# Kernel tuning notes

Measured on AMD Instinct MI355X. Metric: run time of the kernel, lower is better.

Reference implementation:

```python
import jax, jax.numpy as jnp
import numpy as np

DIM = 128
HEADS = 4
DH = 32
SCALE = DH ** -0.5


def _ln(x, g, b):
    m = x.mean(-1, keepdims=True)
    v = x.var(-1, keepdims=True)
    return (x - m) / jnp.sqrt(v + 1e-5) * g + b


def setup_inputs() -> dict:
    key = jax.random.key(0)
    ks = jax.random.split(key, 16)
    B, N, H, W, HK, WK = 2, 6, 48, 48, 24, 24
    d, hd = DIM, HEADS * DH
    p = lambda k, s: (jax.random.normal(k, s, jnp.float32) * 0.02)
    return {
        "q": jax.random.normal(ks[0], (B, N, d, H, W), jnp.float32),
        "k": jax.random.normal(ks[1], (B, N, d, HK, WK), jnp.float32),
        "v": jax.random.normal(ks[2], (B, N, d, HK, WK), jnp.float32),
        "skip": jax.random.normal(ks[3], (B, d, H, W), jnp.float32),
        "lnq_g": jnp.ones(d), "lnq_b": jnp.zeros(d),
        "Wq": p(ks[4], (d, hd)), "bq": jnp.zeros(hd),
        "lnk_g": jnp.ones(d), "lnk_b": jnp.zeros(d),
        "Wk": p(ks[5], (d, hd)), "bk": jnp.zeros(hd),
        "lnv_g": jnp.ones(d), "lnv_b": jnp.zeros(d),
        "Wv": p(ks[6], (d, hd)), "bv": jnp.zeros(hd),
        "Wp": p(ks[7], (hd, d)), "bp": jnp.zeros(d),
        "pre_g": jnp.ones(d), "pre_b": jnp.zeros(d),
        "W1": p(ks[8], (d, 2 * d)), "b1": jnp.zeros(2 * d),
        "W2": p(ks[9], (2 * d, d)), "b2": jnp.zeros(d),
        "post_g": jnp.ones(d), "post_b": jnp.zeros(d),
    }


def reference(q, k, v, skip, lnq_g, lnq_b, Wq, bq, lnk_g, lnk_b, Wk, bk,
              lnv_g, lnv_b, Wv, bv, Wp, bp, pre_g, pre_b, W1, b1, W2, b2,
              post_g, post_b):
    B, N, d, H, W = q.shape
    _, _, _, HK, WK = k.shape
    Q, K = H * W, HK * WK
    # b n d H W -> b n (H W) d
    qx = q.transpose(0, 1, 3, 4, 2).reshape(B, N, Q, d)
    kx = k.transpose(0, 1, 3, 4, 2).reshape(B, N, K, d)
    vx = v.transpose(0, 1, 3, 4, 2).reshape(B, N * K, d)
    # norm + linear projections
    qp = _ln(qx, lnq_g, lnq_b) @ Wq + bq  # (B,N,Q,HEADS*DH)
    kp = _ln(kx, lnk_g, lnk_b) @ Wk + bk
    vp = _ln(vx, lnv_g, lnv_b) @ Wv + bv  # (B,N*K,HEADS*DH)
    # split heads: b ... (m d) -> (b m) ... d
    qp = qp.reshape(B, N, Q, HEADS, DH).transpose(0, 3, 1, 2, 4).reshape(B * HEADS, N, Q, DH)
    kp = kp.reshape(B, N, K, HEADS, DH).transpose(0, 3, 1, 2, 4).reshape(B * HEADS, N, K, DH)
    vp = vp.reshape(B, N * K, HEADS, DH).transpose(0, 2, 1, 3).reshape(B * HEADS, N * K, DH)
    # per-view scores, then softmax jointly over (n K)
    scores = SCALE * jnp.einsum('bnqd,bnkd->bnqk', qp, kp)
    scores = scores.transpose(0, 2, 1, 3).reshape(B * HEADS, Q, N * K)
    a = jax.nn.softmax(scores, axis=-1)
    out = jnp.einsum('bqk,bkd->bqd', a, vp)  # (B*HEADS, Q, DH)
    # merge heads: (b m) Q d -> b Q (m d)
    z = out.reshape(B, HEADS, Q, DH).transpose(0, 2, 1, 3).reshape(B, Q, HEADS * DH)
    z = z @ Wp + bp
    z = z + skip.transpose(0, 2, 3, 1).reshape(B, Q, d)
    z = _ln(z, pre_g, pre_b)
    z = z + (jax.nn.gelu(z @ W1 + b1, approximate=False) @ W2 + b2)
    z = _ln(z, post_g, post_b)
    return z.reshape(B, H, W, d).transpose(0, 3, 1, 2)
```

## Files before the change

### kernel.cpp

```cpp
#include <hip/hip_runtime.h>
#include <cmath>

#define B_    2
#define N_    6
#define D_    128
#define Q_    2304
#define K_    576
#define NK_   3456
#define HEADS_ 4
#define DH_   32
#define SCALE_ 0.17677669529663687f
#define SCLOG2E_ 0.25504672615621814f

typedef __attribute__((ext_vector_type(8))) short bf16x8;
typedef __attribute__((ext_vector_type(4))) float f32x4;

#if defined(__has_builtin)
#if __has_builtin(__builtin_amdgcn_cvt_pk_bf16_f32)
#define HAS_PK_BF16 1
#endif
#endif

static __device__ __forceinline__ unsigned short f2bf(float f) {
  union { float f; unsigned u; } x; x.f = f;
  unsigned u = x.u + 0x7fffu + ((x.u >> 16) & 1u);
  return (unsigned short)(u >> 16);
}
static __device__ __forceinline__ unsigned pkbf(float a, float b) {
#ifdef HAS_PK_BF16
  typedef __attribute__((ext_vector_type(2))) __bf16 vbf2;
  union { vbf2 v; unsigned u; } cv;
  cv.v = __builtin_amdgcn_cvt_pk_bf16_f32(a, b);
  return cv.u;
#else
  return (unsigned)f2bf(a) | ((unsigned)f2bf(b) << 16);
#endif
}

static __device__ __forceinline__ void pl32sw(unsigned &a, unsigned &b) {
  asm("v_permlane32_swap_b32 %0, %1" : "+v"(a), "+v"(b));
}
static __device__ __forceinline__ void pl16sw(unsigned &a, unsigned &b) {
  asm("v_permlane16_swap_b32 %0, %1" : "+v"(a), "+v"(b));
}

__global__ __launch_bounds__(256) void k_prep_wt(
    const float* __restrict__ Wq, const float* __restrict__ Wk,
    const float* __restrict__ Wv, const float* __restrict__ Wp,
    const float* __restrict__ W1, const float* __restrict__ W2,
    unsigned short* __restrict__ WTq, unsigned short* __restrict__ WTk,
    unsigned short* __restrict__ WTv, unsigned short* __restrict__ WTp,
    unsigned short* __restrict__ WT1, unsigned short* __restrict__ WT2,
    float* __restrict__ Z, int zn)
{
  __shared__ float tile[32][33];
  const int wb = blockIdx.x, t = threadIdx.x;
  {
    const float4 z4 = {0.f, 0.f, 0.f, 0.f};
    for (int i = wb * 256 + t; i < zn; i += 128 * 256)
      ((float4*)Z)[i] = z4;
  }
  const float* src; unsigned short* dst; int Kd, J, tl;
  if      (wb < 16) { src = Wq; dst = WTq; Kd = 128; J = 128; tl = wb; }
  else if (wb < 32) { src = Wk; dst = WTk; Kd = 128; J = 128; tl = wb - 16; }
  else if (wb < 48) { src = Wv; dst = WTv; Kd = 128; J = 128; tl = wb - 32; }
  else if (wb < 64) { src = Wp; dst = WTp; Kd = 128; J = 128; tl = wb - 48; }
  else if (wb < 96) { src = W1; dst = WT1; Kd = 128; J = 256; tl = wb - 64; }
  else              { src = W2; dst = WT2; Kd = 256; J = 128; tl = wb - 96; }
  const int njt = J >> 5;
  const int tj = tl % njt, tk = tl / njt;
#pragma unroll
  for (int i = 0; i < 4; ++i) {
    int idx = t + 256 * i;
    int r = idx >> 5, c = idx & 31;
    tile[r][c] = src[(size_t)(tk * 32 + r) * J + tj * 32 + c];
  }
  __syncthreads();
#pragma unroll
  for (int i = 0; i < 2; ++i) {
    int idx = t + 256 * i;
    int rr = idx >> 4, c2 = (idx & 15) << 1;
    *(unsigned*)&dst[(size_t)(tj * 32 + rr) * Kd + tk * 32 + c2] =
        pkbf(tile[c2][rr], tile[c2 + 1][rr]);
  }
}

__global__ __launch_bounds__(256) void k_ln_proj_all(
    const float* __restrict__ qin, const float* __restrict__ kin,
    const float* __restrict__ vin,
    const float* __restrict__ lnq_g, const float* __restrict__ lnq_b,
    const float* __restrict__ lnk_g, const float* __restrict__ lnk_b,
    const float* __restrict__ lnv_g, const float* __restrict__ lnv_b,
    const unsigned short* __restrict__ WTq, const unsigned short* __restrict__ WTk,
    const unsigned short* __restrict__ WTv,
    const float* __restrict__ bq, const float* __restrict__ bk,
    const float* __restrict__ bv,
    unsigned short* __restrict__ QPh, unsigned short* __restrict__ KPh,
    unsigned short* __restrict__ VPTh)
{
  __shared__ float xs[32][132];
  __shared__ unsigned short xh[32][136];
  __shared__ float gs[128], bs[128];
  __shared__ float mu[32], rsd[32];
  const int t = threadIdx.x;
  const int bid = blockIdx.x;

  const float* x; const unsigned short* WT; const float* g; const float* bl;
  const float* bias; int S, blk, mode; float osc;
  if (bid < 864)       { mode = 0; blk = bid;        x = qin; WT = WTq; g = lnq_g; bl = lnq_b; bias = bq; S = Q_; osc = SCLOG2E_; }
  else if (bid < 1080) { mode = 0; blk = bid - 864;  x = kin; WT = WTk; g = lnk_g; bl = lnk_b; bias = bk; S = K_; osc = 1.0f; }
  else                 { mode = 1; blk = bid - 1080; x = vin; WT = WTv; g = lnv_g; bl = lnv_b; bias = bv; S = K_; osc = 1.0f; }
  const int ntile = S >> 5;
  const int o  = blk / ntile;
  const int s0 = (blk % ntile) << 5;

  if (t < 128) { gs[t] = g[t]; bs[t] = bl[t]; }
  const float* xb = x + (size_t)o * 128 * (size_t)S + s0;
#pragma unroll
  for (int i = 0; i < 4; ++i) {
    int idx = t + 256 * i;
    int c = idx >> 3, s4 = (idx & 7) << 2;
    float4 xv = *(const float4*)&xb[(size_t)c * S + s4];
    xs[s4 + 0][c] = xv.x; xs[s4 + 1][c] = xv.y;
    xs[s4 + 2][c] = xv.z; xs[s4 + 3][c] = xv.w;
  }
  __syncthreads();
  {
    int s = t >> 3, l8 = t & 7;
    float sum = 0.f, sq = 0.f;
    for (int c = l8; c < 128; c += 8) { float v = xs[s][c]; sum += v; sq += v * v; }
#pragma unroll
    for (int off = 4; off > 0; off >>= 1) {
      sum += __shfl_down(sum, off, 8);
      sq  += __shfl_down(sq,  off, 8);
    }
    if (l8 == 0) {
      float mth = sum * 0.0078125f;
      float var = sq * 0.0078125f - mth * mth;
      mu[s] = mth; rsd[s] = rsqrtf(var + 1e-5f);
    }
  }
  __syncthreads();
#pragma unroll
  for (int i = 0; i < 8; ++i) {
    int idx = t + 256 * i;
    int s = idx >> 6, c2 = (idx & 63) << 1;
    float y0 = (xs[s][c2]     - mu[s]) * rsd[s] * gs[c2]     + bs[c2];
    float y1 = (xs[s][c2 + 1] - mu[s]) * rsd[s] * gs[c2 + 1] + bs[c2 + 1];
    *(unsigned*)&xh[s][c2] = pkbf(y0, y1);
  }
  __syncthreads();
  const int w = t >> 6, lane = t & 63, quad = lane >> 4, l16 = lane & 15;
  const f32x4 zf = {0.f, 0.f, 0.f, 0.f};
  f32x4 acc[2][2] = {{zf, zf}, {zf, zf}};
#pragma unroll
  for (int kc = 0; kc < 4; ++kc) {
    bf16x8 a0 = *(const bf16x8*)&xh[l16][kc * 32 + quad * 8];
    bf16x8 a1 = *(const bf16x8*)&xh[16 + l16][kc * 32 + quad * 8];
    bf16x8 b0 = *(const bf16x8*)&WT[(size_t)(w * 32 + l16) * 128 + kc * 32 + quad * 8];
    bf16x8 b1 = *(const bf16x8*)&WT[(size_t)(w * 32 + 16 + l16) * 128 + kc * 32 + quad * 8];
    acc[0][0] = __builtin_amdgcn_mfma_f32_16x16x32_bf16(a0, b0, acc[0][0], 0, 0, 0);
    acc[0][1] = __builtin_amdgcn_mfma_f32_16x16x32_bf16(a0, b1, acc[0][1], 0, 0, 0);
    acc[1][0] = __builtin_amdgcn_mfma_f32_16x16x32_bf16(a1, b0, acc[1][0], 0, 0, 0);
    acc[1][1] = __builtin_amdgcn_mfma_f32_16x16x32_bf16(a1, b1, acc[1][1], 0, 0, 0);
  }
  if (mode == 0) {
    unsigned short* outh = (bid < 864) ? QPh : KPh;
    __syncthreads();
#pragma unroll
    for (int mt = 0; mt < 2; ++mt)
#pragma unroll
      for (int nt = 0; nt < 2; ++nt) {
        int col = w * 32 + nt * 16 + l16;
        float bc = bias[col];
#pragma unroll
        for (int r = 0; r < 4; ++r)
          xh[mt * 16 + quad * 4 + r][col] = f2bf((acc[mt][nt][r] + bc) * osc);
      }
    __syncthreads();
#pragma unroll
    for (int i = 0; i < 2; ++i) {
      int s = i * 16 + (t >> 4), c8 = (t & 15) << 3;
      *(uint4*)&outh[((size_t)o * S + s0 + s) * 128 + c8] = *(uint4*)&xh[s][c8];
    }
  } else {
    const int b = o / 6, n = o % 6;
#pragma unroll
    for (int mt = 0; mt < 2; ++mt)
#pragma unroll
      for (int nt = 0; nt < 2; ++nt) {
        int col = w * 32 + nt * 16 + l16;
        int hh = col >> 5, dh = col & 31;
        float bc = bias[col];
        ushort4 pk;
        *(unsigned*)&pk.x = pkbf(acc[mt][nt][0] + bc, acc[mt][nt][1] + bc);
        *(unsigned*)&pk.z = pkbf(acc[mt][nt][2] + bc, acc[mt][nt][3] + bc);
        int s = n * 576 + s0 + mt * 16 + quad * 4;
        *(ushort4*)&VPTh[((size_t)(b * 4 + hh) * 32 + dh) * (size_t)NK_ + s] = pk;
      }
  }
}

__global__ __launch_bounds__(256) void k_attn_mfma(
    const unsigned short* __restrict__ QPh, const unsigned short* __restrict__ KPh,
    const unsigned short* __restrict__ VPTh, float* __restrict__ PO,
    float* __restrict__ Pl)
{
  __shared__ __align__(16) unsigned short smem[2][2048];
  const int t = threadIdx.x;
  const int w = t >> 6, lane = t & 63;
  const int quad = lane >> 4, l16 = lane & 15;
  const int qg  = blockIdx.x % 18;
  const int rest = blockIdx.x / 18;
  const int bhx = rest & 7, nn = rest >> 3;
  const int bb = bhx >> 2, h = bhx & 3;
  const int q0 = (qg * 4 + w) << 5;

  const unsigned short* kb = KPh + ((size_t)(bb * 6 + nn) * K_) * 128 + h * 32;
  const unsigned short* qb = QPh + ((size_t)(bb * 6 + nn) * Q_ + q0) * 128 + h * 32;
  const unsigned short* vb = VPTh + (size_t)bhx * 32 * (size_t)NK_ + (size_t)nn * 18 * 32;

  bf16x8 qc0 = *(const bf16x8*)&qb[(size_t)l16 * 128 + quad * 8];
  bf16x8 qc1 = *(const bf16x8*)&qb[(size_t)(16 + l16) * 128 + quad * 8];

  const int row16 = l16 + ((w & 1) << 4);
  const int xsl = (quad ^ ((l16 >> 1) & 3)) << 3;
  const unsigned short* sbase = (w < 2)
      ? kb + (size_t)row16 * 128 + quad * 8
      : vb + (size_t)row16 * NK_ + quad * 8;
  const int sstride = (w < 2) ? 4096 : 32;
  const int wdst = ((w >= 2) ? 1024 : 0) + row16 * 32 + xsl;

  const f32x4 zf = {0.f, 0.f, 0.f, 0.f};
  f32x4 o00 = zf, o01 = zf, o10 = zf, o11 = zf;
  float lsum0 = 0.f, lsum1 = 0.f;

  uint4 st0 = *(const uint4*)&sbase[0];
  uint4 stn = *(const uint4*)&sbase[sstride];
  *(uint4*)&smem[0][wdst] = st0;
  __syncthreads();

#pragma unroll 2
  for (int kc = 0; kc < 18; ++kc) {
    const int buf = kc & 1;
    if (kc < 17) *(uint4*)&smem[buf ^ 1][wdst] = stn;
    if (kc < 16) stn = *(const uint4*)&sbase[(size_t)(kc + 2) * sstride];

    const unsigned short* sb = &smem[buf][0];
    bf16x8 kf0 = *(const bf16x8*)&sb[l16 * 32 + xsl];
    bf16x8 kf1 = *(const bf16x8*)&sb[(16 + l16) * 32 + xsl];
    bf16x8 pv0 = *(const bf16x8*)&sb[1024 + l16 * 32 + xsl];
    bf16x8 pv1 = *(const bf16x8*)&sb[1024 + (16 + l16) * 32 + xsl];

    __builtin_amdgcn_s_setprio(1);
    f32x4 s00 = __builtin_amdgcn_mfma_f32_16x16x32_bf16(kf0, qc0, zf, 0, 0, 0);
    f32x4 s01 = __builtin_amdgcn_mfma_f32_16x16x32_bf16(kf1, qc0, zf, 0, 0, 0);
    f32x4 s10 = __builtin_amdgcn_mfma_f32_16x16x32_bf16(kf0, qc1, zf, 0, 0, 0);
    f32x4 s11 = __builtin_amdgcn_mfma_f32_16x16x32_bf16(kf1, qc1, zf, 0, 0, 0);

    float a00 = __builtin_amdgcn_exp2f(s00.x), a01 = __builtin_amdgcn_exp2f(s00.y);
    float a02 = __builtin_amdgcn_exp2f(s00.z), a03 = __builtin_amdgcn_exp2f(s00.w);
    float a10 = __builtin_amdgcn_exp2f(s01.x), a11 = __builtin_amdgcn_exp2f(s01.y);
    float a12 = __builtin_amdgcn_exp2f(s01.z), a13 = __builtin_amdgcn_exp2f(s01.w);
    lsum0 += (a00 + a01 + a02 + a03) + (a10 + a11 + a12 + a13);
    float b00 = __builtin_amdgcn_exp2f(s10.x), b01 = __builtin_amdgcn_exp2f(s10.y);
    float b02 = __builtin_amdgcn_exp2f(s10.z), b03 = __builtin_amdgcn_exp2f(s10.w);
    float b10 = __builtin_amdgcn_exp2f(s11.x), b11 = __builtin_amdgcn_exp2f(s11.y);
    float b12 = __builtin_amdgcn_exp2f(s11.z), b13 = __builtin_amdgcn_exp2f(s11.w);
    lsum1 += (b00 + b01 + b02 + b03) + (b10 + b11 + b12 + b13);

    unsigned xA0 = pkbf(a00, a01), xA1 = pkbf(a02, a03);
    unsigned xB0 = pkbf(a10, a11), xB1 = pkbf(a12, a13);
    unsigned yA0 = pkbf(b00, b01), yA1 = pkbf(b02, b03);
    unsigned yB0 = pkbf(b10, b11), yB1 = pkbf(b12, b13);
    pl32sw(xA0, xB0); pl32sw(xA1, xB1);
    pl16sw(xA0, xB0); pl16sw(xA1, xB1);
    pl32sw(yA0, yB0); pl32sw(yA1, yB1);
    pl16sw(yA0, yB0); pl16sw(yA1, yB1);
    union { unsigned u[4]; bf16x8 v; } f0, f1;
    f0.u[0] = xA0; f0.u[1] = xA1; f0.u[2] = xB0; f0.u[3] = xB1;
    f1.u[0] = yA0; f1.u[1] = yA1; f1.u[2] = yB0; f1.u[3] = yB1;

    o00 = __builtin_amdgcn_mfma_f32_16x16x32_bf16(f0.v, pv0, o00, 0, 0, 0);
    o01 = __builtin_amdgcn_mfma_f32_16x16x32_bf16(f0.v, pv1, o01, 0, 0, 0);
    o10 = __builtin_amdgcn_mfma_f32_16x16x32_bf16(f1.v, pv0, o10, 0, 0, 0);
    o11 = __builtin_amdgcn_mfma_f32_16x16x32_bf16(f1.v, pv1, o11, 0, 0, 0);
    __builtin_amdgcn_s_setprio(0);
    __syncthreads();
  }

  lsum0 += __shfl_xor(lsum0, 16);
  lsum0 += __shfl_xor(lsum0, 32);
  lsum1 += __shfl_xor(lsum1, 16);
  lsum1 += __shfl_xor(lsum1, 32);
  if (lane < 16) {
    atomicAdd(&Pl[(size_t)bhx * Q_ + q0 + lane], lsum0);
    atomicAdd(&Pl[(size_t)bhx * Q_ + q0 + 16 + lane], lsum1);
  }
  float* pob = PO + ((size_t)bhx * Q_ + q0) * 32;
#pragma unroll
  for (int r = 0; r < 4; ++r) {
    atomicAdd(&pob[(quad * 4 + r) * 32 + l16],           o00[r]);
    atomicAdd(&pob[(quad * 4 + r) * 32 + 16 + l16],      o01[r]);
    atomicAdd(&pob[(16 + quad * 4 + r) * 32 + l16],      o10[r]);
    atomicAdd(&pob[(16 + quad * 4 + r) * 32 + 16 + l16], o11[r]);
  }
}

__global__ __launch_bounds__(512) void k_tail(
    const float* __restrict__ PO, const float* __restrict__ Pl,
    const unsigned short* __restrict__ WTp, const float* __restrict__ bp,
    const float* __restrict__ skip,
    const float* __restrict__ pre_g, const float* __restrict__ pre_b,
    const unsigned short* __restrict__ WT1, const float* __restrict__ b1,
    const unsigned short* __restrict__ WT2, const float* __restrict__ b2,
    const float* __restrict__ post_g, const float* __restrict__ post_b,
    float* __restrict__ out)
{
  __shared__ float xs[16][132];
  __shared__ unsigned short xh[16][136];
  __shared__ unsigned short hb[16][264];
  __shared__ float g1s[128], b1s[128], g2s[128], b2s[128];
  __shared__ float mu[16], rsd[16];
  const int t = threadIdx.x;
  const int row0 = blockIdx.x << 4;
  const int bb = row0 / Q_, hw0 = row0 % Q_;
  const int w = t >> 6, lane = t & 63, quad = lane >> 4, l16 = lane & 15;
  const f32x4 zf = {0.f, 0.f, 0.f, 0.f};

  if (t < 128) { g1s[t] = pre_g[t]; b1s[t] = pre_b[t]; g2s[t] = post_g[t]; b2s[t] = post_b[t]; }
#pragma unroll
  for (int i = 0; i < 2; ++i) {
    int idx = t + 512 * i;
    int s = idx >> 6, c2 = (idx & 63) << 1;
    int q = hw0 + s;
    int h = c2 >> 5, dh = c2 & 31;
    size_t bq = (size_t)(bb * 4 + h) * Q_ + q;
    size_t i0 = bq * 32 + dh;
    float2 pp = *(const float2*)&PO[i0];
    float inv = 1.f / Pl[bq];
    *(unsigned*)&xh[s][c2] = pkbf(pp.x * inv, pp.y * inv);
  }
  __syncthreads();
  {
    f32x4 acc = zf;
    const int col = w * 16 + l16;
#pragma unroll
    for (int kc = 0; kc < 4; ++kc) {
      bf16x8 a0 = *(const bf16x8*)&xh[l16][kc * 32 + quad * 8];
      bf16x8 b0 = *(const bf16x8*)&WTp[(size_t)col * 128 + kc * 32 + quad * 8];
      acc = __builtin_amdgcn_mfma_f32_16x16x32_bf16(a0, b0, acc, 0, 0, 0);
    }
    float bc = bp[col];
    float4 sk = *(const float4*)&skip[((size_t)bb * 128 + col) * Q_ + hw0 + quad * 4];
    xs[quad * 4 + 0][col] = acc[0] + bc + sk.x;
    xs[quad * 4 + 1][col] = acc[1] + bc + sk.y;
    xs[quad * 4 + 2][col] = acc[2] + bc + sk.z;
    xs[quad * 4 + 3][col] = acc[3] + bc + sk.w;
  }
  __syncthreads();
  {
    int s = t >> 5, lg = t & 31;
    float sum = 0.f, sq = 0.f;
    for (int c = lg; c < 128; c += 32) { float v = xs[s][c]; sum += v; sq += v * v; }
#pragma unroll
    for (int off = 16; off > 0; off >>= 1) {
      sum += __shfl_down(sum, off, 32);
      sq  += __shfl_down(sq,  off, 32);
    }
    if (lg == 0) {
      float mth = sum * 0.0078125f;
      float var = sq * 0.0078125f - mth * mth;
      mu[s] = mth; rsd[s] = rsqrtf(var + 1e-5f);
    }
  }
  __syncthreads();
#pragma unroll
  for (int i = 0; i < 2; ++i) {
    int idx = t + 512 * i;
    int s = idx >> 6, c2 = (idx & 63) << 1;
    float y0 = (xs[s][c2]     - mu[s]) * rsd[s] * g1s[c2]     + b1s[c2];
    float y1 = (xs[s][c2 + 1] - mu[s]) * rsd[s] * g1s[c2 + 1] + b1s[c2 + 1];
    xs[s][c2] = y0; xs[s][c2 + 1] = y1;
    *(unsigned*)&xh[s][c2] = pkbf(y0, y1);
  }
  __syncthreads();
  {
#pragma unroll
    for (int nt = 0; nt < 2; ++nt) {
      const int col = w * 32 + nt * 16 + l16;
      f32x4 acc = zf;
#pragma unroll
      for (int kc = 0; kc < 4; ++kc) {
        bf16x8 a0 = *(const bf16x8*)&xh[l16][kc * 32 + quad * 8];
        bf16x8 b0 = *(const bf16x8*)&WT1[(size_t)col * 128 + kc * 32 + quad * 8];
        acc = __builtin_amdgcn_mfma_f32_16x16x32_bf16(a0, b0, acc, 0, 0, 0);
      }
      float bc = b1[col];
#pragma unroll
      for (int r = 0; r < 4; ++r) {
        float hx = acc[r] + bc;
        hb[quad * 4 + r][col] =
            f2bf(0.5f * hx * (1.f + erff(hx * 0.7071067811865476f)));
      }
    }
  }
  __syncthreads();
  {
    f32x4 acc = zf;
    const int col = w * 16 + l16;
#pragma unroll
    for (int kc = 0; kc < 8; ++kc) {
      bf16x8 a0 = *(const bf16x8*)&hb[l16][kc * 32 + quad * 8];
      bf16x8 b0 = *(const bf16x8*)&WT2[(size_t)col * 256 + kc * 32 + quad * 8];
      acc = __builtin_amdgcn_mfma_f32_16x16x32_bf16(a0, b0, acc, 0, 0, 0);
    }
    float bc = b2[col];
#pragma unroll
    for (int r = 0; r < 4; ++r) {
      int row = quad * 4 + r;
      xs[row][col] = acc[r] + bc + xs[row][col];
    }
  }
  __syncthreads();
  {
    int s = t >> 5, lg = t & 31;
    float sum = 0.f, sq = 0.f;
    for (int c = lg; c < 128; c += 32) { float v = xs[s][c]; sum += v; sq += v * v; }
#pragma unroll
    for (int off = 16; off > 0; off >>= 1) {
      sum += __shfl_down(sum, off, 32);
      sq  += __shfl_down(sq,  off, 32);
    }
    if (lg == 0) {
      float mth = sum * 0.0078125f;
      float var = sq * 0.0078125f - mth * mth;
      mu[s] = mth; rsd[s] = rsqrtf(var + 1e-5f);
    }
  }
  __syncthreads();
#pragma unroll
  for (int i = 0; i < 4; ++i) {
    int idx = t + 512 * i;
    int s = idx & 15, c = idx >> 4;
    out[(size_t)bb * (128 * (size_t)Q_) + (size_t)c * Q_ + hw0 + s] =
        (xs[s][c] - mu[s]) * rsd[s] * g2s[c] + b2s[c];
  }
}

extern "C" void kernel_launch(void* const* d_in, const int* in_sizes, int n_in,
                              void* d_out, int out_size, void* d_ws, size_t ws_size,
                              hipStream_t stream) {
  const float* q     = (const float*)d_in[0];
  const float* k     = (const float*)d_in[1];
  const float* v     = (const float*)d_in[2];
  const float* skip  = (const float*)d_in[3];
  const float* lnq_g = (const float*)d_in[4];
  const float* lnq_b = (const float*)d_in[5];
  const float* Wq    = (const float*)d_in[6];
  const float* bq    = (const float*)d_in[7];
  const float* lnk_g = (const float*)d_in[8];
  const float* lnk_b = (const float*)d_in[9];
  const float* Wk    = (const float*)d_in[10];
  const float* bk    = (const float*)d_in[11];
  const float* lnv_g = (const float*)d_in[12];
  const float* lnv_b = (const float*)d_in[13];
  const float* Wv    = (const float*)d_in[14];
  const float* bvv   = (const float*)d_in[15];
  const float* Wp    = (const float*)d_in[16];
  const float* bp    = (const float*)d_in[17];
  const float* pre_g = (const float*)d_in[18];
  const float* pre_b = (const float*)d_in[19];
  const float* W1    = (const float*)d_in[20];
  const float* b1    = (const float*)d_in[21];
  const float* W2    = (const float*)d_in[22];
  const float* b2    = (const float*)d_in[23];
  const float* post_g= (const float*)d_in[24];
  const float* post_b= (const float*)d_in[25];
  float* out = (float*)d_out;

  unsigned short* QPh  = (unsigned short*)d_ws;
  unsigned short* KPh  = QPh + 3538944;
  unsigned short* VPTh = KPh + 884736;
  float* PO  = (float*)(VPTh + 884736);
  float* Pl  = PO + 589824;
  unsigned short* WTq = (unsigned short*)(Pl + 18432);
  unsigned short* WTk = WTq + 16384;
  unsigned short* WTv = WTk + 16384;
  unsigned short* WTp = WTv + 16384;
  unsigned short* WT1 = WTp + 16384;
  unsigned short* WT2 = WT1 + 32768;
  const int zn = (589824 + 18432) / 4;

  k_prep_wt<<<dim3(128), dim3(256), 0, stream>>>(Wq, Wk, Wv, Wp, W1, W2,
                                                 WTq, WTk, WTv, WTp, WT1, WT2,
                                                 PO, zn);
  k_ln_proj_all<<<dim3(1296), dim3(256), 0, stream>>>(
      q, k, v, lnq_g, lnq_b, lnk_g, lnk_b, lnv_g, lnv_b,
      WTq, WTk, WTv, bq, bk, bvv, QPh, KPh, VPTh);
  k_attn_mfma<<<dim3(18 * 8 * 6), dim3(256), 0, stream>>>(QPh, KPh, VPTh, PO, Pl);
  k_tail<<<dim3(288), dim3(512), 0, stream>>>(PO, Pl, WTp, bp, skip,
                                              pre_g, pre_b, WT1, b1, WT2, b2,
                                              post_g, post_b, out);
}
```

Before: 165.0 us.

## Replace atomic partial-sum accumulation with per-view partial buffers reduced in tail

After: 167.2 us. About the same (+1.4%).

```diff
diff --git a/kernel.cpp b/kernel.cpp
--- a/kernel.cpp
+++ b/kernel.cpp
@@ -50,16 +50,10 @@
     const float* __restrict__ W1, const float* __restrict__ W2,
     unsigned short* __restrict__ WTq, unsigned short* __restrict__ WTk,
     unsigned short* __restrict__ WTv, unsigned short* __restrict__ WTp,
-    unsigned short* __restrict__ WT1, unsigned short* __restrict__ WT2,
-    float* __restrict__ Z, int zn)
+    unsigned short* __restrict__ WT1, unsigned short* __restrict__ WT2)
 {
   __shared__ float tile[32][33];
   const int wb = blockIdx.x, t = threadIdx.x;
-  {
-    const float4 z4 = {0.f, 0.f, 0.f, 0.f};
-    for (int i = wb * 256 + t; i < zn; i += 128 * 256)
-      ((float4*)Z)[i] = z4;
-  }
   const float* src; unsigned short* dst; int Kd, J, tl;
   if      (wb < 16) { src = Wq; dst = WTq; Kd = 128; J = 128; tl = wb; }
   else if (wb < 32) { src = Wk; dst = WTk; Kd = 128; J = 128; tl = wb - 16; }
@@ -206,7 +200,9 @@
     const unsigned short* __restrict__ VPTh, float* __restrict__ PO,
     float* __restrict__ Pl)
 {
-  __shared__ __align__(16) unsigned short smem[2][2048];
+  __shared__ __align__(16) char smem_u[18432];
+  unsigned short (*smem)[2048] = (unsigned short (*)[2048])smem_u;
+  float (*ol)[32][36] = (float (*)[32][36])smem_u;
   const int t = threadIdx.x;
   const int w = t >> 6, lane = t & 63;
   const int quad = lane >> 4, l16 = lane & 15;
@@ -294,16 +290,26 @@
   lsum1 += __shfl_xor(lsum1, 16);
   lsum1 += __shfl_xor(lsum1, 32);
   if (lane < 16) {
-    atomicAdd(&Pl[(size_t)bhx * Q_ + q0 + lane], lsum0);
-    atomicAdd(&Pl[(size_t)bhx * Q_ + q0 + 16 + lane], lsum1);
-  }
-  float* pob = PO + ((size_t)bhx * Q_ + q0) * 32;
+    float* plb = Pl + (size_t)(nn * 8 + bhx) * Q_ + q0;
+    plb[lane]      = lsum0;
+    plb[16 + lane] = lsum1;
+  }
 #pragma unroll
   for (int r = 0; r < 4; ++r) {
-    atomicAdd(&pob[(quad * 4 + r) * 32 + l16],           o00[r]);
-    atomicAdd(&pob[(quad * 4 + r) * 32 + 16 + l16],      o01[r]);
-    atomicAdd(&pob[(16 + quad * 4 + r) * 32 + l16],      o10[r]);
-    atomicAdd(&pob[(16 + quad * 4 + r) * 32 + 16 + l16], o11[r]);
+    ol[w][quad * 4 + r][l16]           = o00[r];
+    ol[w][quad * 4 + r][16 + l16]      = o01[r];
+    ol[w][16 + quad * 4 + r][l16]      = o10[r];
+    ol[w][16 + quad * 4 + r][16 + l16] = o11[r];
+  }
+  __syncthreads();
+  {
+    float* pob = PO + (size_t)(nn * 8 + bhx) * (Q_ * 32) + (size_t)qg * (128 * 32);
+    const int qr = t >> 1, d0 = (t & 1) << 4;
+#pragma unroll
+    for (int j = 0; j < 4; ++j) {
+      float4 vv = *(const float4*)&ol[qr >> 5][qr & 31][d0 + j * 4];
+      *(float4*)&pob[(size_t)t * 16 + j * 4] = vv;
+    }
   }
 }
 
@@ -337,9 +343,15 @@
     int h = c2 >> 5, dh = c2 & 31;
     size_t bq = (size_t)(bb * 4 + h) * Q_ + q;
     size_t i0 = bq * 32 + dh;
-    float2 pp = *(const float2*)&PO[i0];
-    float inv = 1.f / Pl[bq];
-    *(unsigned*)&xh[s][c2] = pkbf(pp.x * inv, pp.y * inv);
+    float px = 0.f, py = 0.f, l = 0.f;
+#pragma unroll
+    for (int p = 0; p < 6; ++p) {
+      float2 pp = *(const float2*)&PO[(size_t)p * 589824 + i0];
+      px += pp.x; py += pp.y;
+      l += Pl[(size_t)p * 18432 + bq];
+    }
+    float inv = 1.f / l;
+    *(unsigned*)&xh[s][c2] = pkbf(px * inv, py * inv);
   }
   __syncthreads();
   {
@@ -483,18 +495,16 @@
   unsigned short* KPh  = QPh + 3538944;
   unsigned short* VPTh = KPh + 884736;
   float* PO  = (float*)(VPTh + 884736);
-  float* Pl  = PO + 589824;
-  unsigned short* WTq = (unsigned short*)(Pl + 18432);
+  float* Pl  = PO + (size_t)6 * 589824;
+  unsigned short* WTq = (unsigned short*)(Pl + (size_t)6 * 18432);
   unsigned short* WTk = WTq + 16384;
   unsigned short* WTv = WTk + 16384;
   unsigned short* WTp = WTv + 16384;
   unsigned short* WT1 = WTp + 16384;
   unsigned short* WT2 = WT1 + 32768;
-  const int zn = (589824 + 18432) / 4;
 
   k_prep_wt<<<dim3(128), dim3(256), 0, stream>>>(Wq, Wk, Wv, Wp, W1, W2,
-                                                 WTq, WTk, WTv, WTp, WT1, WT2,
-                                                 PO, zn);
+                                                 WTq, WTk, WTv, WTp, WT1, WT2);
   k_ln_proj_all<<<dim3(1296), dim3(256), 0, stream>>>(
       q, k, v, lnq_g, lnq_b, lnk_g, lnk_b, lnv_g, lnv_b,
       WTq, WTk, WTv, bq, bk, bvv, QPh, KPh, VPTh);
```

## Split attention keys across two blocks and preload all K/V chunks upfront

Applied to the files above, without the earlier changes.

New measurement: 171.4 us. 3.9% more time.

```diff
diff --git a/kernel.cpp b/kernel.cpp
--- a/kernel.cpp
+++ b/kernel.cpp
@@ -206,88 +206,97 @@
     const unsigned short* __restrict__ VPTh, float* __restrict__ PO,
     float* __restrict__ Pl)
 {
-  __shared__ __align__(16) unsigned short smem[2][2048];
+  __shared__ __align__(16) unsigned short kv[9][2048];
   const int t = threadIdx.x;
   const int w = t >> 6, lane = t & 63;
   const int quad = lane >> 4, l16 = lane & 15;
   const int qg  = blockIdx.x % 18;
   const int rest = blockIdx.x / 18;
-  const int bhx = rest & 7, nn = rest >> 3;
+  const int bhx = rest & 7;
+  const int rest2 = rest >> 3;
+  const int nn = rest2 >> 1, half = rest2 & 1;
   const int bb = bhx >> 2, h = bhx & 3;
   const int q0 = (qg * 4 + w) << 5;
 
   const unsigned short* kb = KPh + ((size_t)(bb * 6 + nn) * K_) * 128 + h * 32;
   const unsigned short* qb = QPh + ((size_t)(bb * 6 + nn) * Q_ + q0) * 128 + h * 32;
-  const unsigned short* vb = VPTh + (size_t)bhx * 32 * (size_t)NK_ + (size_t)nn * 18 * 32;
+  const unsigned short* vb = VPTh + (size_t)bhx * 32 * (size_t)NK_
+                             + (size_t)nn * 18 * 32 + (size_t)half * 288;
 
   bf16x8 qc0 = *(const bf16x8*)&qb[(size_t)l16 * 128 + quad * 8];
   bf16x8 qc1 = *(const bf16x8*)&qb[(size_t)(16 + l16) * 128 + quad * 8];
 
-  const int row16 = l16 + ((w & 1) << 4);
-  const int xsl = (quad ^ ((l16 >> 1) & 3)) << 3;
-  const unsigned short* sbase = (w < 2)
-      ? kb + (size_t)row16 * 128 + quad * 8
-      : vb + (size_t)row16 * NK_ + quad * 8;
-  const int sstride = (w < 2) ? 4096 : 32;
-  const int wdst = ((w >= 2) ? 1024 : 0) + row16 * 32 + xsl;
-
+  {
+    const int sr = (t & 127) >> 2, sc = t & 3;
+    const int isV = t >> 7;
+    const unsigned short* gsrc; size_t gstep;
+    if (!isV) { gsrc = kb + (size_t)(half * 288 + sr) * 128 + sc * 8; gstep = 32 * 128; }
+    else      { gsrc = vb + (size_t)sr * NK_ + sc * 8;                gstep = 32; }
+    const int ldst = isV * 1024 + sr * 32 + ((sc ^ ((sr >> 1) & 3)) << 3);
+    uint4 stg0 = *(const uint4*)&gsrc[0];
+    uint4 stg1 = *(const uint4*)&gsrc[gstep];
+    uint4 stg2 = *(const uint4*)&gsrc[2 * gstep];
+    uint4 stg3 = *(const uint4*)&gsrc[3 * gstep];
+    uint4 stg4 = *(const uint4*)&gsrc[4 * gstep];
+    uint4 stg5 = *(const uint4*)&gsrc[5 * gstep];
+    uint4 stg6 = *(const uint4*)&gsrc[6 * gstep];
+    uint4 stg7 = *(const uint4*)&gsrc[7 * gstep];
+    uint4 stg8 = *(const uint4*)&gsrc[8 * gstep];
+    *(uint4*)&kv[0][ldst] = stg0;
+    *(uint4*)&kv[1][ldst] = stg1;
+    *(uint4*)&kv[2][ldst] = stg2;
+    *(uint4*)&kv[3][ldst] = stg3;
+    *(uint4*)&kv[4][ldst] = stg4;
+    *(uint4*)&kv[5][ldst] = stg5;
+    *(uint4*)&kv[6][ldst] = stg6;
+    *(uint4*)&kv[7][ldst] = stg7;
+    *(uint4*)&kv[8][ldst] = stg8;
+  }
+  __syncthreads();
+
+  const int krd = l16 * 32 + ((quad ^ ((l16 >> 1) & 3)) << 3);
   const f32x4 zf = {0.f, 0.f, 0.f, 0.f};
   f32x4 o00 = zf, o01 = zf, o10 = zf, o11 = zf;
   float lsum0 = 0.f, lsum1 = 0.f;
 
-  uint4 st0 = *(const uint4*)&sbase[0];
-  uint4 stn = *(const uint4*)&sbase[sstride];
-  *(uint4*)&smem[0][wdst] = st0;
-  __syncthreads();
-
-#pragma unroll 2
-  for (int kc = 0; kc < 18; ++kc) {
-    const int buf = kc & 1;
-    if (kc < 17) *(uint4*)&smem[buf ^ 1][wdst] = stn;
-    if (kc < 16) stn = *(const uint4*)&sbase[(size_t)(kc + 2) * sstride];
-
-    const unsigned short* sb = &smem[buf][0];
-    bf16x8 kf0 = *(const bf16x8*)&sb[l16 * 32 + xsl];
-    bf16x8 kf1 = *(const bf16x8*)&sb[(16 + l16) * 32 + xsl];
-    bf16x8 pv0 = *(const bf16x8*)&sb[1024 + l16 * 32 + xsl];
-    bf16x8 pv1 = *(const bf16x8*)&sb[1024 + (16 + l16) * 32 + xsl];
+#define MKFRAG(sA, sB, ls, fr) { \
+    float e0 = __builtin_amdgcn_exp2f(sA.x), e1 = __builtin_amdgcn_exp2f(sA.y); \
+    float e2 = __builtin_amdgcn_exp2f(sA.z), e3 = __builtin_amdgcn_exp2f(sA.w); \
+    float e4 = __builtin_amdgcn_exp2f(sB.x), e5 = __builtin_amdgcn_exp2f(sB.y); \
+    float e6 = __builtin_amdgcn_exp2f(sB.z), e7 = __builtin_amdgcn_exp2f(sB.w); \
+    ls += (e0 + e1 + e2 + e3) + (e4 + e5 + e6 + e7); \
+    unsigned A0 = pkbf(e0, e1), A1 = pkbf(e2, e3); \
+    unsigned B0 = pkbf(e4, e5), B1 = pkbf(e6, e7); \
+    pl32sw(A0, B0); pl32sw(A1, B1); pl16sw(A0, B0); pl16sw(A1, B1); \
+    fr.u[0] = A0; fr.u[1] = A1; fr.u[2] = B0; fr.u[3] = B1; }
+
+#pragma unroll 3
+  for (int cc = 0; cc < 9; ++cc) {
+    const unsigned short* sb = kv[cc];
+    bf16x8 kf0 = *(const bf16x8*)&sb[krd];
+    bf16x8 kf1 = *(const bf16x8*)&sb[krd + 512];
+    bf16x8 pv0 = *(const bf16x8*)&sb[1024 + krd];
+    bf16x8 pv1 = *(const bf16x8*)&sb[1024 + krd + 512];
 
     __builtin_amdgcn_s_setprio(1);
     f32x4 s00 = __builtin_amdgcn_mfma_f32_16x16x32_bf16(kf0, qc0, zf, 0, 0, 0);
     f32x4 s01 = __builtin_amdgcn_mfma_f32_16x16x32_bf16(kf1, qc0, zf, 0, 0, 0);
     f32x4 s10 = __builtin_amdgcn_mfma_f32_16x16x32_bf16(kf0, qc1, zf, 0, 0, 0);
     f32x4 s11 = __builtin_amdgcn_mfma_f32_16x16x32_bf16(kf1, qc1, zf, 0, 0, 0);
-
-    float a00 = __builtin_amdgcn_exp2f(s00.x), a01 = __builtin_amdgcn_exp2f(s00.y);
-    float a02 = __builtin_amdgcn_exp2f(s00.z), a03 = __builtin_amdgcn_exp2f(s00.w);
-    float a10 = __builtin_amdgcn_exp2f(s01.x), a11 = __builtin_amdgcn_exp2f(s01.y);
-    float a12 = __builtin_amdgcn_exp2f(s01.z), a13 = __builtin_amdgcn_exp2f(s01.w);
-    lsum0 += (a00 + a01 + a02 + a03) + (a10 + a11 + a12 + a13);
-    float b00 = __builtin_amdgcn_exp2f(s10.x), b01 = __builtin_amdgcn_exp2f(s10.y);
-    float b02 = __builtin_amdgcn_exp2f(s10.z), b03 = __builtin_amdgcn_exp2f(s10.w);
-    float b10 = __builtin_amdgcn_exp2f(s11.x), b11 = __builtin_amdgcn_exp2f(s11.y);
-    float b12 = __builtin_amdgcn_exp2f(s11.z), b13 = __builtin_amdgcn_exp2f(s11.w);
-    lsum1 += (b00 + b01 + b02 + b03) + (b10 + b11 + b12 + b13);
-
-    unsigned xA0 = pkbf(a00, a01), xA1 = pkbf(a02, a03);
-    unsigned xB0 = pkbf(a10, a11), xB1 = pkbf(a12, a13);
-    unsigned yA0 = pkbf(b00, b01), yA1 = pkbf(b02, b03);
-    unsigned yB0 = pkbf(b10, b11), yB1 = pkbf(b12, b13);
-    pl32sw(xA0, xB0); pl32sw(xA1, xB1);
-    pl16sw(xA0, xB0); pl16sw(xA1, xB1);
-    pl32sw(yA0, yB0); pl32sw(yA1, yB1);
-    pl16sw(yA0, yB0); pl16sw(yA1, yB1);
+    __builtin_amdgcn_s_setprio(0);
+
     union { unsigned u[4]; bf16x8 v; } f0, f1;
-    f0.u[0] = xA0; f0.u[1] = xA1; f0.u[2] = xB0; f0.u[3] = xB1;
-    f1.u[0] = yA0; f1.u[1] = yA1; f1.u[2] = yB0; f1.u[3] = yB1;
-
+    MKFRAG(s00, s01, lsum0, f0);
+    MKFRAG(s10, s11, lsum1, f1);
+
+    __builtin_amdgcn_s_setprio(1);
     o00 = __builtin_amdgcn_mfma_f32_16x16x32_bf16(f0.v, pv0, o00, 0, 0, 0);
     o01 = __builtin_amdgcn_mfma_f32_16x16x32_bf16(f0.v, pv1, o01, 0, 0, 0);
     o10 = __builtin_amdgcn_mfma_f32_16x16x32_bf16(f1.v, pv0, o10, 0, 0, 0);
     o11 = __builtin_amdgcn_mfma_f32_16x16x32_bf16(f1.v, pv1, o11, 0, 0, 0);
     __builtin_amdgcn_s_setprio(0);
-    __syncthreads();
-  }
+  }
+#undef MKFRAG
 
   lsum0 += __shfl_xor(lsum0, 16);
   lsum0 += __shfl_xor(lsum0, 32);
@@ -498,7 +507,7 @@
   k_ln_proj_all<<<dim3(1296), dim3(256), 0, stream>>>(
       q, k, v, lnq_g, lnq_b, lnk_g, lnk_b, lnv_g, lnv_b,
       WTq, WTk, WTv, bq, bk, bvv, QPh, KPh, VPTh);
-  k_attn_mfma<<<dim3(18 * 8 * 6), dim3(256), 0, stream>>>(QPh, KPh, VPTh, PO, Pl);
+  k_attn_mfma<<<dim3(1728), dim3(256), 0, stream>>>(QPh, KPh, VPTh, PO, Pl);
   k_tail<<<dim3(288), dim3(512), 0, stream>>>(PO, Pl, WTp, bp, skip,
                                               pre_g, pre_b, WT1, b1, WT2, b2,
                                               post_g, post_b, out);
```

## Split attention key range in halves across blocks and compute row sums via MFMA

Applied to the files above, without the earlier changes.

New measurement: 174.2 us. 5.6% more time.

```diff
diff --git a/kernel.cpp b/kernel.cpp
--- a/kernel.cpp
+++ b/kernel.cpp
@@ -212,13 +212,16 @@
   const int quad = lane >> 4, l16 = lane & 15;
   const int qg  = blockIdx.x % 18;
   const int rest = blockIdx.x / 18;
-  const int bhx = rest & 7, nn = rest >> 3;
+  const int bhx = rest & 7;
+  const int rest2 = rest >> 3;
+  const int nn = rest2 >> 1, half = rest2 & 1;
   const int bb = bhx >> 2, h = bhx & 3;
   const int q0 = (qg * 4 + w) << 5;
 
-  const unsigned short* kb = KPh + ((size_t)(bb * 6 + nn) * K_) * 128 + h * 32;
+  const unsigned short* kb = KPh + ((size_t)(bb * 6 + nn) * K_ + half * 288) * 128 + h * 32;
   const unsigned short* qb = QPh + ((size_t)(bb * 6 + nn) * Q_ + q0) * 128 + h * 32;
-  const unsigned short* vb = VPTh + (size_t)bhx * 32 * (size_t)NK_ + (size_t)nn * 18 * 32;
+  const unsigned short* vb = VPTh + (size_t)bhx * 32 * (size_t)NK_
+                             + (size_t)nn * 576 + half * 288;
 
   bf16x8 qc0 = *(const bf16x8*)&qb[(size_t)l16 * 128 + quad * 8];
   bf16x8 qc1 = *(const bf16x8*)&qb[(size_t)(16 + l16) * 128 + quad * 8];
@@ -233,18 +236,21 @@
 
   const f32x4 zf = {0.f, 0.f, 0.f, 0.f};
   f32x4 o00 = zf, o01 = zf, o10 = zf, o11 = zf;
-  float lsum0 = 0.f, lsum1 = 0.f;
+  f32x4 accl0 = zf, accl1 = zf;
+  bf16x8 onesb;
+#pragma unroll
+  for (int i = 0; i < 8; ++i) onesb[i] = (short)0x3F80;
 
   uint4 st0 = *(const uint4*)&sbase[0];
   uint4 stn = *(const uint4*)&sbase[sstride];
   *(uint4*)&smem[0][wdst] = st0;
   __syncthreads();
 
-#pragma unroll 2
-  for (int kc = 0; kc < 18; ++kc) {
+#pragma unroll 3
+  for (int kc = 0; kc < 9; ++kc) {
     const int buf = kc & 1;
-    if (kc < 17) *(uint4*)&smem[buf ^ 1][wdst] = stn;
-    if (kc < 16) stn = *(const uint4*)&sbase[(size_t)(kc + 2) * sstride];
+    if (kc < 8) *(uint4*)&smem[buf ^ 1][wdst] = stn;
+    if (kc < 7) stn = *(const uint4*)&sbase[(size_t)(kc + 2) * sstride];
 
     const unsigned short* sb = &smem[buf][0];
     bf16x8 kf0 = *(const bf16x8*)&sb[l16 * 32 + xsl];
@@ -262,12 +268,10 @@
     float a02 = __builtin_amdgcn_exp2f(s00.z), a03 = __builtin_amdgcn_exp2f(s00.w);
     float a10 = __builtin_amdgcn_exp2f(s01.x), a11 = __builtin_amdgcn_exp2f(s01.y);
     float a12 = __builtin_amdgcn_exp2f(s01.z), a13 = __builtin_amdgcn_exp2f(s01.w);
-    lsum0 += (a00 + a01 + a02 + a03) + (a10 + a11 + a12 + a13);
     float b00 = __builtin_amdgcn_exp2f(s10.x), b01 = __builtin_amdgcn_exp2f(s10.y);
     float b02 = __builtin_amdgcn_exp2f(s10.z), b03 = __builtin_amdgcn_exp2f(s10.w);
     float b10 = __builtin_amdgcn_exp2f(s11.x), b11 = __builtin_amdgcn_exp2f(s11.y);
     float b12 = __builtin_amdgcn_exp2f(s11.z), b13 = __builtin_amdgcn_exp2f(s11.w);
-    lsum1 += (b00 + b01 + b02 + b03) + (b10 + b11 + b12 + b13);
 
     unsigned xA0 = pkbf(a00, a01), xA1 = pkbf(a02, a03);
     unsigned xB0 = pkbf(a10, a11), xB1 = pkbf(a12, a13);
@@ -285,17 +289,19 @@
     o01 = __builtin_amdgcn_mfma_f32_16x16x32_bf16(f0.v, pv1, o01, 0, 0, 0);
     o10 = __builtin_amdgcn_mfma_f32_16x16x32_bf16(f1.v, pv0, o10, 0, 0, 0);
     o11 = __builtin_amdgcn_mfma_f32_16x16x32_bf16(f1.v, pv1, o11, 0, 0, 0);
+    accl0 = __builtin_amdgcn_mfma_f32_16x16x32_bf16(f0.v, onesb, accl0, 0, 0, 0);
+    accl1 = __builtin_amdgcn_mfma_f32_16x16x32_bf16(f1.v, onesb, accl1, 0, 0, 0);
     __builtin_amdgcn_s_setprio(0);
     __syncthreads();
   }
 
-  lsum0 += __shfl_xor(lsum0, 16);
-  lsum0 += __shfl_xor(lsum0, 32);
-  lsum1 += __shfl_xor(lsum1, 16);
-  lsum1 += __shfl_xor(lsum1, 32);
-  if (lane < 16) {
-    atomicAdd(&Pl[(size_t)bhx * Q_ + q0 + lane], lsum0);
-    atomicAdd(&Pl[(size_t)bhx * Q_ + q0 + 16 + lane], lsum1);
+  if (l16 == 0) {
+    float* plb = Pl + (size_t)bhx * Q_ + q0;
+#pragma unroll
+    for (int r = 0; r < 4; ++r) {
+      atomicAdd(&plb[quad * 4 + r],      accl0[r]);
+      atomicAdd(&plb[16 + quad * 4 + r], accl1[r]);
+    }
   }
   float* pob = PO + ((size_t)bhx * Q_ + q0) * 32;
 #pragma unroll
@@ -498,7 +504,7 @@
   k_ln_proj_all<<<dim3(1296), dim3(256), 0, stream>>>(
       q, k, v, lnq_g, lnq_b, lnk_g, lnk_b, lnv_g, lnv_b,
       WTq, WTk, WTv, bq, bk, bvv, QPh, KPh, VPTh);
-  k_attn_mfma<<<dim3(18 * 8 * 6), dim3(256), 0, stream>>>(QPh, KPh, VPTh, PO, Pl);
+  k_attn_mfma<<<dim3(18 * 8 * 12), dim3(256), 0, stream>>>(QPh, KPh, VPTh, PO, Pl);
   k_tail<<<dim3(288), dim3(512), 0, stream>>>(PO, Pl, WTp, bp, skip,
                                               pre_g, pre_b, WT1, b1, WT2, b2,
                                               post_g, post_b, out);
```
